# Optimization experiments

Hardware: AMD Instinct MI355X
Metric: run time of the kernel (lower is better)

## Reference

```python
import jax, jax.numpy as jnp
import numpy as np

B, S, D = 2, 1024, 512
E, K = 8, 2          # num_experts, top_k (hardcoded in EncoderLayerMOE)
HMOE = 4             # SMoE_MHA heads
HD = D // HMOE       # 128 head dim for local experts
HID = 4 * D          # 2048 expert hidden (both extractors)
AH = 4               # attention heads
DK = D // AH
NEG = -1e9


def layer_norm(x, w, b, eps=1e-12):
    mu = x.mean(-1, keepdims=True)
    var = ((x - mu) ** 2).mean(-1, keepdims=True)
    return (x - mu) * jax.lax.rsqrt(var + eps) * w + b


def moe(x, gate_w, gate_b, w1, b1, w2, b2):
    """Dense all-expert SMoE, gather top-k, re-softmax topk weights (faithful).
    x: [..., d]; w1: [E,d,H]; w2: [E,H,d]."""
    gate_scores = x @ gate_w + gate_b                      # [..., E]
    sm = jax.nn.softmax(gate_scores, axis=-1)
    topk_s, topk_i = jax.lax.top_k(sm, K)                  # [..., K]
    h1 = jax.nn.relu(jnp.einsum('...d,edh->...eh', x, w1) + b1)   # [..., E, H]
    out = jnp.einsum('...eh,ehd->...ed', h1, w2) + b2      # [..., E, d]
    idx = jnp.broadcast_to(topk_i[..., None], topk_i.shape + (out.shape[-1],))
    sel = jnp.take_along_axis(out, idx, axis=-2)           # [..., K, d]
    w = jax.nn.softmax(topk_s, axis=-1)[..., None]         # re-softmax of topk scores
    return (sel * w).sum(-2)


def local_extractor(x, pre_w, pre_b, gate_w, gate_b, w1, b1, w2, b2, align_w, align_b):
    b, s, d = x.shape
    xp = x @ pre_w + pre_b
    xf = xp.reshape(b, s, HMOE, HD).transpose(0, 2, 1, 3)  # [b,h,s,hd]
    eo = moe(xf, gate_w, gate_b, w1, b1, w2, b2)
    xf = xf + eo
    xo = xf.transpose(0, 2, 1, 3).reshape(b, s, d)
    return xo @ align_w + align_b


def mha(xq, xkv, mask, wq, bq, wk, bk, wv, bv, wo, bo):
    b, sq, d = xq.shape
    sk = xkv.shape[1]
    q = (xq @ wq + bq).reshape(b, sq, AH, DK).transpose(0, 2, 1, 3)
    k = (xkv @ wk + bk).reshape(b, sk, AH, DK).transpose(0, 2, 1, 3)
    v = (xkv @ wv + bv).reshape(b, sk, AH, DK).transpose(0, 2, 1, 3)
    scores = jnp.einsum('bhqd,bhkd->bhqk', q, k) / jnp.sqrt(jnp.float32(DK))
    m = mask[:, None, :, :]                                 # [b,1,1,sk]
    scores = jnp.where(m, scores, NEG)
    attn = jax.nn.softmax(scores, axis=-1)
    attn = jnp.where(m, attn, 0.0)
    o = jnp.einsum('bhqk,bhkd->bhqd', attn, v)
    o = o.transpose(0, 2, 1, 3).reshape(b, sq, d)
    return o @ wo + bo


def setup_inputs() -> dict:
    key = jax.random.key(0)
    ks = iter(jax.random.split(key, 64))
    def p(shape, scale=0.02):
        return (jax.random.normal(next(ks), shape, jnp.float32) * scale)
    z = lambda *s: jnp.zeros(s, jnp.float32)
    o = lambda *s: jnp.ones(s, jnp.float32)
    return dict(
        x=jax.random.normal(next(ks), (B, S, D), jnp.float32),
        pre_w=p((D, D)), pre_b=z(D),
        l_gate_w=p((HD, E)), l_gate_b=z(E),
        l_w1=p((E, HD, HID)), l_b1=z(E, HID),
        l_w2=p((E, HID, HD)), l_b2=z(E, HD),
        align_w=p((D, D)), align_b=z(D),
        ln1_w=o(D), ln1_b=z(D),
        wq=p((D, D)), bq=z(D), wk=p((D, D)), bk=z(D),
        wv=p((D, D)), bv=z(D), wo=p((D, D)), bo=z(D),
        ln2_w=o(D), ln2_b=z(D),
        g_gate_w=p((D, E)), g_gate_b=z(E),
        g_w1=p((E, D, HID)), g_b1=z(E, HID),
        g_w2=p((E, HID, D)), g_b2=z(E, D),
        mask=jnp.ones((B, 1, S), bool),
    )


def reference(x, pre_w, pre_b, l_gate_w, l_gate_b, l_w1, l_b1, l_w2, l_b2,
              align_w, align_b, ln1_w, ln1_b, wq, bq, wk, bk, wv, bv, wo, bo,
              ln2_w, ln2_b, g_gate_w, g_gate_b, g_w1, g_b1, g_w2, g_b2, mask):
    # EncoderLayerMOE.forward, eval mode, normalize_before=True, cache=None
    residual = x
    xl = local_extractor(x, pre_w, pre_b, l_gate_w, l_gate_b,
                         l_w1, l_b1, l_w2, l_b2, align_w, align_b)
    xn = layer_norm(xl, ln1_w, ln1_b)
    att = mha(xn, xn, mask, wq, bq, wk, bk, wv, bv, wo, bo)
    x1 = residual + att
    residual = x1
    x2 = layer_norm(x1, ln2_w, ln2_b)
    g = moe(x2, g_gate_w, g_gate_b, g_w1, g_b1, g_w2, g_b2)
    out = residual + g
    return out
```

## Files before the change

### kernel.cpp

```cpp
#include <hip/hip_runtime.h>

typedef unsigned short ushort_t;
typedef __attribute__((ext_vector_type(8))) short short8;
typedef __attribute__((ext_vector_type(4))) short short4v;
typedef __attribute__((ext_vector_type(4))) float f32x4;

constexpr int B_    = 2;
constexpr int S_    = 1024;
constexpr int D_    = 512;
constexpr int E_    = 8;
constexpr int HMOE_ = 4;
constexpr int HD_   = 128;
constexpr int HID_  = 2048;
constexpr int AH_   = 4;
constexpr int NTOK  = B_ * S_;
constexpr int NSUB  = B_ * HMOE_ * S_;

#define DEVINL __device__ __forceinline__

DEVINL ushort_t f2bf(float f) {
    union { float f; unsigned int i; } c;
    c.f = f;
    unsigned int x = c.i;
    return (ushort_t)((x + 0x7fffu + ((x >> 16) & 1u)) >> 16);
// ... 146 lines not shown

__global__ __launch_bounds__(256) void wconv_k(
    const float* __restrict__ in, ushort_t* __restrict__ out, int R, int C)
{
    __shared__ float tile[64][65];
    const int e = blockIdx.z;
    const int c0 = blockIdx.x * 64, r0 = blockIdx.y * 64;
    const float* src = in + ((size_t)e * R + r0) * C + c0;
    const int cl = threadIdx.x & 63, rl = threadIdx.x >> 6;
    #pragma unroll
    for (int j = 0; j < 16; j++) {
        int rr = rl * 16 + j;
        tile[rr][cl] = src[(size_t)rr * C + cl];
    }
    __syncthreads();
    ushort_t* dst = out + ((size_t)e * C + c0) * R + r0;
    #pragma unroll
    for (int j = 0; j < 16; j++) {
        int cc = rl * 16 + j;
        dst[(size_t)cc * R + cl] = f2bf(tile[cl][cc]);
    }
}

__global__ __launch_bounds__(256) void f2bf_k(
    const float* __restrict__ X, ushort_t* __restrict__ Y, int n)
{
    int i = (blockIdx.x * 256 + threadIdx.x) * 4;
    if (i < n) {
        float4 v = *reinterpret_cast<const float4*>(X + i);
        short4v o;
        o.x = (short)f2bf(v.x); o.y = (short)f2bf(v.y);
        o.z = (short)f2bf(v.z); o.w = (short)f2bf(v.w);
        *reinterpret_cast<short4v*>(Y + i) = o;
    }
}

__global__ __launch_bounds__(256) void vtrans_bf_k(
    const ushort_t* __restrict__ Vbf, ushort_t* __restrict__ VT)
{
    __shared__ ushort_t tile[64][68];
    const int s0 = blockIdx.x * 64;
    const int d0 = blockIdx.y * 64;
    const int bh = blockIdx.z;
    const int b = bh >> 2, h = bh & 3;
    const ushort_t* src = Vbf + (size_t)(b * S_ + s0) * D_ + h * HD_ + d0;
    const int cl = threadIdx.x & 63, rl = threadIdx.x >> 6;
    #pragma unroll
    for (int j = 0; j < 16; j++) {
        int rr = rl * 16 + j;
        tile[rr][cl] = src[(size_t)rr * D_ + cl];
    }
    __syncthreads();
    ushort_t* dst = VT + ((size_t)bh * HD_ + d0) * S_ + s0;
    #pragma unroll
    for (int j = 0; j < 16; j++) {
        int cc = rl * 16 + j;
        dst[(size_t)cc * S_ + cl] = tile[cl][cc];
    }
}

template <bool LOCAL>
__global__ __launch_bounds__(256) void gate_score_k(
    const float* __restrict__ X, const float* __restrict__ gwm,
    const float* __restrict__ gb, int2* __restrict__ choice,
    float2* __restrict__ cweight)
{
    constexpr int DIMD = LOCAL ? HD_ : D_;
    constexpr int PL = DIMD / 64;
    const int t = blockIdx.x * 4 + (threadIdx.x >> 6);
    const int lane = threadIdx.x & 63;
    const float* x = X + (LOCAL ? local_off(t) : (size_t)t * D_);
    float xr[PL];
    #pragma unroll
    for (int i = 0; i < PL; i++) xr[i] = x[lane + 64 * i];
    float sc[8];
    #pragma unroll
    for (int e = 0; e < 8; e++) {
        float a = 0.f;
        #pragma unroll
        for (int i = 0; i < PL; i++)
            a = fmaf(xr[i], gwm[(size_t)(lane + 64 * i) * E_ + e], a);
        #pragma unroll
        for (int o2 = 32; o2; o2 >>= 1) a += __shfl_xor(a, o2);
        sc[e] = a;
    }
    if (lane == 0) {
        float mx = -1e30f;
        #pragma unroll
        for (int e = 0; e < 8; e++) { sc[e] += gb[e]; mx = fmaxf(mx, sc[e]); }
        float p[8], psum = 0.f;
        #pragma unroll
        for (int e = 0; e < 8; e++) { p[e] = expf(sc[e] - mx); psum += p[e]; }
        float inv = 1.f / psum;
        #pragma unroll
        for (int e = 0; e < 8; e++) p[e] *= inv;
        int i0 = 0;
        for (int e = 1; e < 8; e++) if (p[e] > p[i0]) i0 = e;
        int i1 = (i0 == 0) ? 1 : 0;
        for (int e = 0; e < 8; e++) if (e != i0 && p[e] > p[i1]) i1 = e;
        float e0 = expf(p[i0]), e1 = expf(p[i1]);
        float wnorm = 1.f / (e0 + e1);
        choice[t]  = (int2){i0, i1};
        cweight[t] = (float2){e0 * wnorm, e1 * wnorm};
    }
}

template <int CAP>
__global__ __launch_bounds__(256) void gate_build_k(
    const int2* __restrict__ choice, const float2* __restrict__ cweight,
    int* __restrict__ cnt, int* __restrict__ idx, float* __restrict__ gwv)
{
    __shared__ int wtot[4];
    __shared__ int basesh;
    const int e = blockIdx.x;
    const int tid = threadIdx.x;
    const int lane = tid & 63, wv = tid >> 6;
    if (tid == 0) basesh = 0;
    __syncthreads();
    for (int t0 = 0; t0 < CAP; t0 += 256) {
        int t = t0 + tid;
        int2 ch = choice[t];
        float2 cw = cweight[t];
        bool m0 = (ch.x == e);
        bool m = m0 | (ch.y == e);
        float w = m0 ? cw.x : cw.y;
        unsigned long long mask = __ballot(m);
        int posw = __popcll(mask & ((1ull << lane) - 1ull));
        if (lane == 0) wtot[wv] = __popcll(mask);
        __syncthreads();
        int base = basesh;
        int woff = 0, tot = 0;
        #pragma unroll
        for (int i = 0; i < 4; i++) {
            int c = wtot[i];
            tot += c;
            if (i < wv) woff += c;
        }
        if (m) {
            int p = base + woff + posw;
            idx[e * CAP + p] = t;
            gwv[e * CAP + p] = w;
        }
        __syncthreads();
        if (tid == 0) basesh = base + tot;
    }
    __syncthreads();
    int total = basesh;
    if (tid == 0) cnt[e] = total;
    int padEnd = (total + 63) & ~63;
    if (padEnd > CAP) padEnd = CAP;
    for (int p = total + tid; p < padEnd; p += 256) {
        idx[e * CAP + p] = 0;
        gwv[e * CAP + p] = 0.f;
    }
}

template <int DIMD, int GSPLIT>
__global__ __launch_bounds__(256, 3) void ffn_grouped3_k(
    const ushort_t* __restrict__ Xbf,
    const ushort_t* __restrict__ w1t, const float* __restrict__ b1,
    const ushort_t* __restrict__ w2t, const float* __restrict__ b2,
    const int* __restrict__ cnt, const int* __restrict__ idx,
    const float* __restrict__ gwv, float* __restrict__ OUT)
{
    constexpr int K1  = DIMD;
    constexpr int NT2 = DIMD / 128;
    constexpr int CAP = (DIMD == HD_) ? NSUB : NTOK;
    constexpr int HC  = 128;
    constexpr int CHUNKS = HID_ / HC / GSPLIT;
    constexpr bool PIPE = (NT2 == 1);

    __shared__ ushort_t bufA[64 * 72];
    __shared__ ushort_t bufB[128 * 72];
    __shared__ ushort_t Hs[64 * 136];
    __shared__ float    gws[64];
    __shared__ size_t   toffs[64];

    const int tid  = threadIdx.x;
    const int lane = tid & 63;
    const int wv   = tid >> 6;
    const int e    = blockIdx.x & 7;
    const int rest = blockIdx.x >> 3;
    const int mt   = rest / GSPLIT;
    const int g    = rest % GSPLIT;
    const int m0   = mt * 64;

    if (m0 >= cnt[e]) return;

    if (tid < 64) {
        int t = idx[e * CAP + m0 + tid];
        toffs[tid] = (DIMD == HD_) ? local_off(t) : (size_t)t * D_;
        gws[tid]   = gwv[e * CAP + m0 + tid];
    }
    __syncthreads();

    const int l15 = lane & 15, l4 = lane >> 4;
    const int ar = tid >> 2, as = (tid & 3) * 16;
    const int bn = tid >> 1, bs = (tid & 1) * 32;

    f32x4 accO[NT2][4][2];
    #pragma unroll
    for (int n2 = 0; n2 < NT2; n2++)
        #pragma unroll
        for (int mi = 0; mi < 4; mi++)
            #pragma unroll
            for (int ni = 0; ni < 2; ni++)
                accO[n2][mi][ni] = (f32x4){0.f, 0.f, 0.f, 0.f};

    const ushort_t* w1e = w1t + (size_t)e * HID_ * K1;
    const ushort_t* w2e = w2t + (size_t)e * DIMD * HID_;
    const float* b1e = b1 + (size_t)e * HID_;

    short8 ra0, ra1, rb0, rb1, rb2, rb3;

    const int hc0 = g * CHUNKS * HC;
    for (int hc = hc0; hc < hc0 + CHUNKS * HC; hc += HC) {
        f32x4 acc1[4][2];
        #pragma unroll
        for (int mi = 0; mi < 4; mi++)
            #pragma unroll
            for (int ni = 0; ni < 2; ni++)
                acc1[mi][ni] = (f32x4){0.f, 0.f, 0.f, 0.f};

        if (PIPE) {
            const ushort_t* xp = Xbf + toffs[ar] + as;
            ra0 = *reinterpret_cast<const short8*>(xp);
            ra1 = *reinterpret_cast<const short8*>(xp + 8);
            const ushort_t* wp = w1e + (size_t)(hc + bn) * K1 + bs;
            rb0 = *reinterpret_cast<const short8*>(wp);
            rb1 = *reinterpret_cast<const short8*>(wp + 8);
            rb2 = *reinterpret_cast<const short8*>(wp + 16);
            rb3 = *reinterpret_cast<const short8*>(wp + 24);
        }

        for (int k0 = 0; k0 < K1; k0 += 64) {
            __syncthreads();
            if (PIPE) {
                ushort_t* dst = &bufA[ar * 72 + as];
                *reinterpret_cast<short8*>(dst)     = ra0;
                *reinterpret_cast<short8*>(dst + 8) = ra1;
                ushort_t* dstb = &bufB[bn * 72 + bs];
                *reinterpret_cast<short8*>(dstb)      = rb0;
                *reinterpret_cast<short8*>(dstb + 8)  = rb1;
                *reinterpret_cast<short8*>(dstb + 16) = rb2;
                *reinterpret_cast<short8*>(dstb + 24) = rb3;
                if (k0 + 64 < K1) {
                    const ushort_t* xp = Xbf + toffs[ar] + k0 + 64 + as;
                    ra0 = *reinterpret_cast<const short8*>(xp);
                    ra1 = *reinterpret_cast<const short8*>(xp + 8);
                    const ushort_t* wp = w1e + (size_t)(hc + bn) * K1 + k0 + 64 + bs;
                    rb0 = *reinterpret_cast<const short8*>(wp);
                    rb1 = *reinterpret_cast<const short8*>(wp + 8);
                    rb2 = *reinterpret_cast<const short8*>(wp + 16);
                    rb3 = *reinterpret_cast<const short8*>(wp + 24);
                }
            } else {
                {
                    const ushort_t* xp = Xbf + toffs[ar] + k0 + as;
                    ushort_t* dst = &bufA[ar * 72 + as];
                    *reinterpret_cast<short8*>(dst)     = *reinterpret_cast<const short8*>(xp);
                    *reinterpret_cast<short8*>(dst + 8) = *reinterpret_cast<const short8*>(xp + 8);
                }
                {
                    const ushort_t* wp = w1e + (size_t)(hc + bn) * K1 + k0 + bs;
                    ushort_t* dst = &bufB[bn * 72 + bs];
                    #pragma unroll
                    for (int j = 0; j < 32; j += 8)
                        *reinterpret_cast<short8*>(dst + j) = *reinterpret_cast<const short8*>(wp + j);
                }
            }
            __syncthreads();
            #pragma unroll
            for (int ks = 0; ks < 2; ks++) {
                short8 af[4], bfr[2];
                #pragma unroll
                for (int mi = 0; mi < 4; mi++)
                    af[mi] = *reinterpret_cast<const short8*>(&bufA[(mi * 16 + l15) * 72 + ks * 32 + l4 * 8]);
                #pragma unroll
                for (int ni = 0; ni < 2; ni++)
                    bfr[ni] = *reinterpret_cast<const short8*>(&bufB[(wv * 32 + ni * 16 + l15) * 72 + ks * 32 + l4 * 8]);
                #pragma unroll
                for (int mi = 0; mi < 4; mi++)
                    #pragma unroll
                    for (int ni = 0; ni < 2; ni++)
                        acc1[mi][ni] = __builtin_amdgcn_mfma_f32_16x16x32_bf16(
                            af[mi], bfr[ni], acc1[mi][ni], 0, 0, 0);
            }
        }

        if (PIPE) {
            const ushort_t* wp = w2e + (size_t)bn * HID_ + hc + bs;
            rb0 = *reinterpret_cast<const short8*>(wp);
            rb1 = *reinterpret_cast<const short8*>(wp + 8);
            rb2 = *reinterpret_cast<const short8*>(wp + 16);
            rb3 = *reinterpret_cast<const short8*>(wp + 24);
        }

        float b1v0 = b1e[hc + wv * 32 + l15];
        float b1v1 = b1e[hc + wv * 32 + 16 + l15];
        #pragma unroll
        for (int mi = 0; mi < 4; mi++)
            #pragma unroll
            for (int ni = 0; ni < 2; ni++) {
                float bb = (ni == 0) ? b1v0 : b1v1;
                #pragma unroll
                for (int r = 0; r < 4; r++) {
                    int row = mi * 16 + l4 * 4 + r;
                    int col = wv * 32 + ni * 16 + l15;
                    Hs[row * 136 + col] = f2bf(fmaxf(acc1[mi][ni][r] + bb, 0.f));
                }
            }

        #pragma unroll
        for (int n2 = 0; n2 < NT2; n2++) {
            #pragma unroll
            for (int k2t = 0; k2t < 2; k2t++) {
                __syncthreads();
                if (PIPE) {
                    ushort_t* dst = &bufB[bn * 72 + bs];
                    *reinterpret_cast<short8*>(dst)      = rb0;
                    *reinterpret_cast<short8*>(dst + 8)  = rb1;
                    *reinterpret_cast<short8*>(dst + 16) = rb2;
                    *reinterpret_cast<short8*>(dst + 24) = rb3;
                    if (!(n2 == NT2 - 1 && k2t == 1)) {
                        int nn2 = (k2t == 1) ? n2 + 1 : n2;
                        int nk  = (k2t == 1) ? 0 : 1;
                        const ushort_t* wp = w2e + (size_t)(nn2 * 128 + bn) * HID_ + hc + nk * 64 + bs;
                        rb0 = *reinterpret_cast<const short8*>(wp);
                        rb1 = *reinterpret_cast<const short8*>(wp + 8);
                        rb2 = *reinterpret_cast<const short8*>(wp + 16);
                        rb3 = *reinterpret_cast<const short8*>(wp + 24);
                    }
                } else {
                    const ushort_t* wp = w2e + (size_t)(n2 * 128 + bn) * HID_ + hc + k2t * 64 + bs;
                    ushort_t* dst = &bufB[bn * 72 + bs];
                    #pragma unroll
                    for (int j = 0; j < 32; j += 8)
                        *reinterpret_cast<short8*>(dst + j) = *reinterpret_cast<const short8*>(wp + j);
                }
                __syncthreads();
                #pragma unroll
                for (int ks = 0; ks < 2; ks++) {
                    short8 af[4], bfr[2];
                    #pragma unroll
                    for (int mi = 0; mi < 4; mi++)
                        af[mi] = *reinterpret_cast<const short8*>(&Hs[(mi * 16 + l15) * 136 + k2t * 64 + ks * 32 + l4 * 8]);
                    #pragma unroll
                    for (int ni = 0; ni < 2; ni++)
                        bfr[ni] = *reinterpret_cast<const short8*>(&bufB[(wv * 32 + ni * 16 + l15) * 72 + ks * 32 + l4 * 8]);
                    #pragma unroll
                    for (int mi = 0; mi < 4; mi++)
                        #pragma unroll
                        for (int ni = 0; ni < 2; ni++)
                            accO[n2][mi][ni] = __builtin_amdgcn_mfma_f32_16x16x32_bf16(
                                af[mi], bfr[ni], accO[n2][mi][ni], 0, 0, 0);
                }
            }
        }
    }

    #pragma unroll
    for (int n2 = 0; n2 < NT2; n2++) {
        float b2v0 = (g == 0) ? b2[(size_t)e * DIMD + n2 * 128 + wv * 32 + l15] : 0.f;
        float b2v1 = (g == 0) ? b2[(size_t)e * DIMD + n2 * 128 + wv * 32 + 16 + l15] : 0.f;
        #pragma unroll
        for (int mi = 0; mi < 4; mi++)
            #pragma unroll
            for (int r = 0; r < 4; r++) {
                int row = mi * 16 + l4 * 4 + r;
                float gg = gws[row];
                if (gg != 0.f) {
                    float* op = OUT + toffs[row] + n2 * 128 + wv * 32;
                    atomicAdd(op + l15,      gg * (accO[n2][mi][0][r] + b2v0));
                    atomicAdd(op + 16 + l15, gg * (accO[n2][mi][1][r] + b2v1));
                }
            }
    }
}

template <int DIMD>
__global__ __launch_bounds__(256) void ffn_grouped_k(
    const float* __restrict__ Xf,
    const float* __restrict__ w1f, const float* __restrict__ b1,
    const float* __restrict__ w2f, const float* __restrict__ b2,
    const int* __restrict__ cnt, const int* __restrict__ idx,
    const float* __restrict__ gwv, float* __restrict__ OUT)
{
    constexpr int K1  = DIMD;
    constexpr int NT2 = DIMD / 128;
    constexpr int CAP = (DIMD == HD_) ? NSUB : NTOK;
    constexpr int HC  = 128;

    __shared__ ushort_t bufB[128 * 72];
    __shared__ ushort_t bufA[128 * 72];
    __shared__ ushort_t Hs[64 * 136];
    __shared__ float    gws[64];
    __shared__ size_t   toffs[64];

    const int tid  = threadIdx.x;
    const int lane = tid & 63;
    const int wv   = tid >> 6;
    const int e    = blockIdx.x & 7;
    const int rest = blockIdx.x >> 3;
    const int mt   = (NT2 == 1) ? rest : (rest >> 2);
    const int n2b  = (NT2 == 1) ? 0 : (rest & 3) * 128;
    const int m0   = mt * 64;

    if (m0 >= cnt[e]) return;

    if (tid < 64) {
        int t = idx[e * CAP + m0 + tid];
        toffs[tid] = (DIMD == HD_) ? local_off(t) : (size_t)t * D_;
        gws[tid]   = gwv[e * CAP + m0 + tid];
    }
    __syncthreads();

    const int l15 = lane & 15, l4 = lane >> 4;

    f32x4 accO[4][2];
    #pragma unroll
    for (int mi = 0; mi < 4; mi++)
        #pragma unroll
        for (int ni = 0; ni < 2; ni++)
            accO[mi][ni] = (f32x4){0.f, 0.f, 0.f, 0.f};

    const float* w1e_f = w1f + (size_t)e * K1 * HID_;
    const float* w2e_f = w2f + (size_t)e * HID_ * DIMD;
    const float* b1e = b1 + (size_t)e * HID_;

    for (int hc = 0; hc < HID_; hc += HC) {
        f32x4 acc1[4][2];
        #pragma unroll
        for (int mi = 0; mi < 4; mi++)
            #pragma unroll
            for (int ni = 0; ni < 2; ni++)
                acc1[mi][ni] = (f32x4){0.f, 0.f, 0.f, 0.f};

        for (int k0 = 0; k0 < K1; k0 += 64) {
            __syncthreads();
            {
                int r = tid >> 2, sg = (tid & 3) * 16;
                const float* xp = Xf + toffs[r] + k0 + sg;
                ushort_t* dst = &bufA[r * 72 + sg];
                #pragma unroll
                for (int j = 0; j < 16; j += 4) {
                    float4 v = *reinterpret_cast<const float4*>(xp + j);
                    dst[j + 0] = f2bf(v.x); dst[j + 1] = f2bf(v.y);
                    dst[j + 2] = f2bf(v.z); dst[j + 3] = f2bf(v.w);
                }
            }
            {
                int kk = tid >> 2, ns = (tid & 3) * 32;
                const float* wp = w1e_f + (size_t)(k0 + kk) * HID_ + hc + ns;
                #pragma unroll
                for (int j = 0; j < 32; j += 4) {
                    float4 v = *reinterpret_cast<const float4*>(wp + j);
                    bufB[(ns + j + 0) * 72 + kk] = f2bf(v.x);
                    bufB[(ns + j + 1) * 72 + kk] = f2bf(v.y);
                    bufB[(ns + j + 2) * 72 + kk] = f2bf(v.z);
                    bufB[(ns + j + 3) * 72 + kk] = f2bf(v.w);
                }
            }
            __syncthreads();
            #pragma unroll
            for (int ks = 0; ks < 2; ks++) {
                short8 af[4], bfr[2];
                #pragma unroll
                for (int mi = 0; mi < 4; mi++)
                    af[mi] = *reinterpret_cast<const short8*>(&bufA[(mi * 16 + l15) * 72 + ks * 32 + l4 * 8]);
                #pragma unroll
                for (int ni = 0; ni < 2; ni++)
                    bfr[ni] = *reinterpret_cast<const short8*>(&bufB[(wv * 32 + ni * 16 + l15) * 72 + ks * 32 + l4 * 8]);
                #pragma unroll
                for (int mi = 0; mi < 4; mi++)
                    #pragma unroll
                    for (int ni = 0; ni < 2; ni++)
                        acc1[mi][ni] = __builtin_amdgcn_mfma_f32_16x16x32_bf16(
                            af[mi], bfr[ni], acc1[mi][ni], 0, 0, 0);
            }
        }

        float b1v0 = b1e[hc + wv * 32 + l15];
        float b1v1 = b1e[hc + wv * 32 + 16 + l15];
        #pragma unroll
        for (int mi = 0; mi < 4; mi++)
            #pragma unroll
            for (int ni = 0; ni < 2; ni++) {
                float bb = (ni == 0) ? b1v0 : b1v1;
                #pragma unroll
                for (int r = 0; r < 4; r++) {
                    int row = mi * 16 + l4 * 4 + r;
                    int col = wv * 32 + ni * 16 + l15;
                    Hs[row * 136 + col] = f2bf(fmaxf(acc1[mi][ni][r] + bb, 0.f));
                }
            }

        #pragma unroll
        for (int k2t = 0; k2t < 2; k2t++) {
            __syncthreads();
            {
                int kk = tid >> 2, ns = (tid & 3) * 32;
                const float* wp = w2e_f + (size_t)(hc + k2t * 64 + kk) * DIMD + n2b + ns;
                #pragma unroll
                for (int j = 0; j < 32; j += 4) {
                    float4 v = *reinterpret_cast<const float4*>(wp + j);
                    bufA[(ns + j + 0) * 72 + kk] = f2bf(v.x);
                    bufA[(ns + j + 1) * 72 + kk] = f2bf(v.y);
                    bufA[(ns + j + 2) * 72 + kk] = f2bf(v.z);
                    bufA[(ns + j + 3) * 72 + kk] = f2bf(v.w);
                }
            }
            __syncthreads();
            #pragma unroll
            for (int ks = 0; ks < 2; ks++) {
                short8 af[4], bfr[2];
                #pragma unroll
                for (int mi = 0; mi < 4; mi++)
                    af[mi] = *reinterpret_cast<const short8*>(&Hs[(mi * 16 + l15) * 136 + k2t * 64 + ks * 32 + l4 * 8]);
                #pragma unroll
                for (int ni = 0; ni < 2; ni++)
                    bfr[ni] = *reinterpret_cast<const short8*>(&bufA[(wv * 32 + ni * 16 + l15) * 72 + ks * 32 + l4 * 8]);
                #pragma unroll
                for (int mi = 0; mi < 4; mi++)
                    #pragma unroll
                    for (int ni = 0; ni < 2; ni++)
                        accO[mi][ni] = __builtin_amdgcn_mfma_f32_16x16x32_bf16(
                            af[mi], bfr[ni], accO[mi][ni], 0, 0, 0);
            }
        }
    }

    float b2v0 = b2[(size_t)e * DIMD + n2b + wv * 32 + l15];
// ... 189 lines not shown

    for (int kc = 0; kc < S_; kc += KC) {
        for (int i = tid * 4; i < KC * 128; i += 1024) {
            int r = i >> 7, c = i & 127;
            float4 v = *reinterpret_cast<const float4*>(Kb + base + (size_t)(kc + r) * D_ + c);
            kst[c + 0][r] = v.x; kst[c + 1][r] = v.y;
            kst[c + 2][r] = v.z; kst[c + 3][r] = v.w;
        }
        __syncthreads();

        {
            float s[2][4] = {};
            #pragma unroll 8
            for (int d = 0; d < 128; d++) {
                float a0 = qsT[d][sy * 2];
                float a1 = qsT[d][sy * 2 + 1];
                float4 kb4 = *reinterpret_cast<const float4*>(&kst[d][sx * 4]);
                s[0][0] = fmaf(a0, kb4.x, s[0][0]); s[0][1] = fmaf(a0, kb4.y, s[0][1]);
                s[0][2] = fmaf(a0, kb4.z, s[0][2]); s[0][3] = fmaf(a0, kb4.w, s[0][3]);
                s[1][0] = fmaf(a1, kb4.x, s[1][0]); s[1][1] = fmaf(a1, kb4.y, s[1][1]);
                s[1][2] = fmaf(a1, kb4.z, s[1][2]); s[1][3] = fmaf(a1, kb4.w, s[1][3]);
            }
            #pragma unroll
            for (int j = 0; j < 4; j++) {
                psT[sx * 4 + j][sy * 2]     = s[0][j];
                psT[sx * 4 + j][sy * 2 + 1] = s[1][j];
            }
        }
        __syncthreads();

        {
            int r = tid >> 3, c0 = (tid & 7) * 8;
            float vals[8];
            float mx = -1e30f;
            #pragma unroll
            for (int j = 0; j < 8; j++) { vals[j] = psT[c0 + j][r]; mx = fmaxf(mx, vals[j]); }
            mx = fmaxf(mx, __shfl_xor(mx, 1));
            mx = fmaxf(mx, __shfl_xor(mx, 2));
            mx = fmaxf(mx, __shfl_xor(mx, 4));
            float mold = mrow[r];
            float mnew = fmaxf(mold, mx);
            float alpha = __expf(mold - mnew);
            float sum = 0.f;
            #pragma unroll
            for (int j = 0; j < 8; j++) {
                float pexp = __expf(vals[j] - mnew);
                psT[c0 + j][r] = pexp;
                sum += pexp;
            }
            sum += __shfl_xor(sum, 1);
            sum += __shfl_xor(sum, 2);
            sum += __shfl_xor(sum, 4);
            if ((tid & 7) == 0) { mrow[r] = mnew; lrow[r] = lrow[r] * alpha + sum; arow[r] = alpha; }
        }
        __syncthreads();

        {
            #pragma unroll
            for (int i2 = 0; i2 < 4; i2++) {
                float al = arow[py * 4 + i2];
                #pragma unroll
                for (int j = 0; j < 4; j++) o[i2][j] *= al;
            }
            #pragma unroll 4
            for (int k = 0; k < KC; k++) {
                float4 pv = *reinterpret_cast<const float4*>(&psT[k][py * 4]);
                float4 vv = *reinterpret_cast<const float4*>(V + base + (size_t)(kc + k) * D_ + px * 4);
                float pa[4] = {pv.x, pv.y, pv.z, pv.w};
                #pragma unroll
                for (int i2 = 0; i2 < 4; i2++) {
                    o[i2][0] = fmaf(pa[i2], vv.x, o[i2][0]);
                    o[i2][1] = fmaf(pa[i2], vv.y, o[i2][1]);
                    o[i2][2] = fmaf(pa[i2], vv.z, o[i2][2]);
                    o[i2][3] = fmaf(pa[i2], vv.w, o[i2][3]);
                }
            }
        }
        __syncthreads();
    }

    #pragma unroll
    for (int i2 = 0; i2 < 4; i2++) {
        float inv = 1.f / lrow[py * 4 + i2];
        float4 ov;
        ov.x = o[i2][0] * inv; ov.y = o[i2][1] * inv;
        ov.z = o[i2][2] * inv; ov.w = o[i2][3] * inv;
        *reinterpret_cast<float4*>(AO + base + (size_t)(q0 + py * 4 + i2) * D_ + px * 4) = ov;
    }
}

__global__ __launch_bounds__(256) void copy_out_k(
    const float* __restrict__ X, float* __restrict__ Y, int n)
{
    int base = (blockIdx.x * 256 + threadIdx.x) * 4;
    if (base < n)
        *reinterpret_cast<float4*>(Y + base) = *reinterpret_cast<const float4*>(X + base);
}

extern "C" void kernel_launch(void* const* d_in, const int* in_sizes, int n_in,
                              void* d_out, int out_size, void* d_ws, size_t ws_size,
                              hipStream_t stream)
{
    (void)in_sizes; (void)n_in; (void)out_size;
    const float* x        = (const float*)d_in[0];
    const float* pre_w    = (const float*)d_in[1];
    const float* pre_b    = (const float*)d_in[2];
    const float* l_gate_w = (const float*)d_in[3];
    const float* l_gate_b = (const float*)d_in[4];
    const float* l_w1     = (const float*)d_in[5];
    const float* l_b1     = (const float*)d_in[6];
    const float* l_w2     = (const float*)d_in[7];
    const float* l_b2     = (const float*)d_in[8];
    const float* align_w  = (const float*)d_in[9];
    const float* align_b  = (const float*)d_in[10];
    const float* ln1_w    = (const float*)d_in[11];
    const float* ln1_b    = (const float*)d_in[12];
    const float* wq       = (const float*)d_in[13];
    const float* bq       = (const float*)d_in[14];
    const float* wk       = (const float*)d_in[15];
    const float* bk       = (const float*)d_in[16];
    const float* wv       = (const float*)d_in[17];
    const float* bv       = (const float*)d_in[18];
    const float* wo       = (const float*)d_in[19];
    const float* bo       = (const float*)d_in[20];
    const float* ln2_w    = (const float*)d_in[21];
    const float* ln2_b    = (const float*)d_in[22];
    const float* g_gate_w = (const float*)d_in[23];
    const float* g_gate_b = (const float*)d_in[24];
    const float* g_w1     = (const float*)d_in[25];
    const float* g_b1     = (const float*)d_in[26];
    const float* g_w2     = (const float*)d_in[27];
    const float* g_b2     = (const float*)d_in[28];

    char* ws = (char*)d_ws;
    const size_t MB  = 1024 * 1024;
    const size_t MB4 = (size_t)NTOK * D_ * sizeof(float);
    float* W0 = (float*)(ws + 0 * MB);
    float* W1 = (float*)(ws + 4 * MB);
    float* W2 = (float*)(ws + 8 * MB);

    const bool pre = ws_size >= (size_t)59 * MB;

    char* blob = ws + (pre ? 12 : 16) * MB;
    int*    cntl = (int*)(blob);
    int*    cntg = (int*)(blob + 32);
    int*    idxl = (int*)(blob + 64);
    int*    idxg = (int*)(blob + 64 + 262144);
    float*  gwvl = (float*)(blob + 64 + 262144 + 65536);
    float*  gwvg = (float*)(blob + 64 + 262144 + 65536 + 262144);
    int2*   chl  = (int2*)(blob + 64 + 262144 + 65536 + 262144 + 65536);
    float2* cwl  = (float2*)((char*)chl + 65536);
    int2*   chg  = (int2*)((char*)cwl + 65536);
    float2* cwg  = (float2*)((char*)chg + 16384);

    ushort_t* x_bf = (ushort_t*)(ws + 12 * MB);
    ushort_t* preT   = (ushort_t*)(ws + 14 * MB);
    ushort_t* alignT = (ushort_t*)(ws + 14 * MB + 512 * 1024);
    ushort_t* wqT    = (ushort_t*)(ws + 15 * MB);
    ushort_t* wkT    = (ushort_t*)(ws + 15 * MB + 512 * 1024);
    ushort_t* wvT    = (ushort_t*)(ws + 16 * MB);
    ushort_t* woT    = (ushort_t*)(ws + 16 * MB + 512 * 1024);
    ushort_t* XBF  = (ushort_t*)(ws + 17 * MB);
    ushort_t* Vbf  = (ushort_t*)(ws + 4 * MB);
    ushort_t* VTb  = (ushort_t*)(ws + 6 * MB);
    ushort_t* Qbf  = (ushort_t*)(ws + 8 * MB);
    ushort_t* Kbf  = (ushort_t*)(ws + 10 * MB);
    ushort_t* LW1T = (ushort_t*)(ws + 19 * MB);
    ushort_t* LW2T = (ushort_t*)(ws + 23 * MB);
    ushort_t* GW1T = (ushort_t*)(ws + 27 * MB);
    ushort_t* GW2T = (ushort_t*)(ws + 43 * MB);
    float* W3 = (float*)(ws + 12 * MB);

    const dim3 gg(D_ / 64, NTOK / 64);

    if (pre) {
        f2bf_k<<<(NTOK * D_) / (256 * 4), 256, 0, stream>>>(x, x_bf, NTOK * D_);
        wconv_k<<<dim3(8, 8, 1), 256, 0, stream>>>(pre_w,   preT,   D_, D_);
        wconv_k<<<dim3(8, 8, 1), 256, 0, stream>>>(align_w, alignT, D_, D_);
        wconv_k<<<dim3(8, 8, 1), 256, 0, stream>>>(wq, wqT, D_, D_);
        wconv_k<<<dim3(8, 8, 1), 256, 0, stream>>>(wk, wkT, D_, D_);
        wconv_k<<<dim3(8, 8, 1), 256, 0, stream>>>(wv, wvT, D_, D_);
        wconv_k<<<dim3(8, 8, 1), 256, 0, stream>>>(wo, woT, D_, D_);
        wconv_k<<<dim3(HID_ / 64, HD_ / 64, 8),  256, 0, stream>>>(l_w1, LW1T, HD_,  HID_);
        wconv_k<<<dim3(HD_ / 64,  HID_ / 64, 8), 256, 0, stream>>>(l_w2, LW2T, HID_, HD_);
        wconv_k<<<dim3(HID_ / 64, D_ / 64, 8),   256, 0, stream>>>(g_w1, GW1T, D_,   HID_);
        wconv_k<<<dim3(D_ / 64,   HID_ / 64, 8), 256, 0, stream>>>(g_w2, GW2T, HID_, D_);

        gemm_mfma_k<true, true, false><<<gg, 256, 0, stream>>>(x_bf, preT, pre_b, nullptr, W0, XBF);
        gate_score_k<true><<<NSUB / 4, 256, 0, stream>>>(W0, l_gate_w, l_gate_b, chl, cwl);
        gate_build_k<NSUB><<<8, 256, 0, stream>>>(chl, cwl, cntl, idxl, gwvl);
        hipMemcpyAsync(W1, W0, MB4, hipMemcpyDeviceToDevice, stream);
        ffn_grouped3_k<HD_, 4><<<8 * (NSUB / 64) * 4, 256, 0, stream>>>(
            XBF, LW1T, l_b1, LW2T, l_b2, cntl, idxl, gwvl, W1);
        f2bf_k<<<(NTOK * D_) / (256 * 4), 256, 0, stream>>>(W1, XBF, NTOK * D_);
        gemm_mfma_k<true, false, false><<<gg, 256, 0, stream>>>(XBF, alignT, align_b, nullptr, W2, nullptr);
        ln_k<false, true><<<NTOK, 256, 0, stream>>>(W2, ln1_w, ln1_b, W0, XBF);
        gemm_mfma_k<false, true, false><<<gg, 256, 0, stream>>>(XBF, wqT, bq, nullptr, nullptr, Qbf);
        gemm_mfma_k<false, true, false><<<gg, 256, 0, stream>>>(XBF, wkT, bk, nullptr, nullptr, Kbf);
        gemm_mfma_k<false, true, false><<<gg, 256, 0, stream>>>(XBF, wvT, bv, nullptr, nullptr, Vbf);
        vtrans_bf_k<<<dim3(16, 2, 8), 256, 0, stream>>>(Vbf, VTb);
        fattn_mfma_k<<<dim3(S_ / 32, B_ * AH_), 256, 0, stream>>>(Qbf, Kbf, VTb, XBF);
        gemm_mfma_k<true, false, true><<<gg, 256, 0, stream>>>(XBF, woT, bo, x, W0, nullptr);
        ln_k<true, true><<<NTOK, 256, 0, stream>>>(W0, ln2_w, ln2_b, W2, XBF);
        gate_score_k<false><<<NTOK / 4, 256, 0, stream>>>(W2, g_gate_w, g_gate_b, chg, cwg);
        gate_build_k<NTOK><<<8, 256, 0, stream>>>(chg, cwg, cntg, idxg, gwvg);
        ffn_grouped3_k<D_, 8><<<8 * (NTOK / 64) * 8, 256, 0, stream>>>(
            XBF, GW1T, g_b1, GW2T, g_b2, cntg, idxg, gwvg, W0);
        copy_out_k<<<(NTOK * D_) / (256 * 4), 256, 0, stream>>>(W0, (float*)d_out, NTOK * D_);
    } else {
        gemm_bias_k<false><<<gg, 256, 0, stream>>>(x, pre_w, pre_b, nullptr, W0, NTOK, D_, D_);
        gate_score_k<true><<<NSUB / 4, 256, 0, stream>>>(W0, l_gate_w, l_gate_b, chl, cwl);
        gate_build_k<NSUB><<<8, 256, 0, stream>>>(chl, cwl, cntl, idxl, gwvl);
        hipMemcpyAsync(W1, W0, MB4, hipMemcpyDeviceToDevice, stream);
        ffn_grouped_k<HD_><<<8 * (NSUB / 64), 256, 0, stream>>>(
            W0, l_w1, l_b1, l_w2, l_b2, cntl, idxl, gwvl, W1);
        gemm_bias_k<false><<<gg, 256, 0, stream>>>(W1, align_w, align_b, nullptr, W2, NTOK, D_, D_);
        ln_k<true, false><<<NTOK, 256, 0, stream>>>(W2, ln1_w, ln1_b, W0, nullptr);
        gemm_bias_k<false><<<gg, 256, 0, stream>>>(W0, wq, bq, nullptr, W1, NTOK, D_, D_);
        gemm_bias_k<false><<<gg, 256, 0, stream>>>(W0, wk, bk, nullptr, W2, NTOK, D_, D_);
        gemm_bias_k<false><<<gg, 256, 0, stream>>>(W0, wv, bv, nullptr, W3, NTOK, D_, D_);
        fattn_k<<<dim3(S_ / QT, B_ * AH_), 256, 0, stream>>>(W1, W2, W3, W1);
        gemm_bias_k<true><<<gg, 256, 0, stream>>>(W1, wo, bo, x, W0, NTOK, D_, D_);
        ln_k<true, false><<<NTOK, 256, 0, stream>>>(W0, ln2_w, ln2_b, W2, nullptr);
        gate_score_k<false><<<NTOK / 4, 256, 0, stream>>>(W2, g_gate_w, g_gate_b, chg, cwg);
        gate_build_k<NTOK><<<8, 256, 0, stream>>>(chg, cwg, cntg, idxg, gwvg);
        ffn_grouped_k<D_><<<8 * (NTOK / 64) * 4, 256, 0, stream>>>(
            W2, g_w1, g_b1, g_w2, g_b2, cntg, idxg, gwvg, W0);
        copy_out_k<<<(NTOK * D_) / (256 * 4), 256, 0, stream>>>(W0, (float*)d_out, NTOK * D_);
    }
}
```

Measured before the change: 507.8 us.

## Split global MoE FFN into two-stage grouped GEMMs with materialized hidden buffer

Replaces the fused per-expert FFN kernel for the global MoE with separate up-projection and down-projection grouped GEMM kernels. A prefix kernel computes per-expert slot offsets, and the ReLU hidden activations are stored in bf16 to a workspace buffer in two 1024-wide hidden halves. The intent is to drop the recompute and GSPLIT partitioning of the fused kernel and improve tile occupancy. In exchange it adds global-memory traffic for the hidden buffer, extra launches, and a second round of atomic adds into the output.

```diff
diff --git a/kernel.cpp b/kernel.cpp
--- a/kernel.cpp
+++ b/kernel.cpp
@@ -322,6 +322,14 @@
     for (int p = total + tid; p < padEnd; p += 256) {
         idx[e * CAP + p] = 0;
         gwv[e * CAP + p] = 0.f;
+    }
+}
+
+__global__ void prefix_k(const int* __restrict__ cnt, int* __restrict__ prefix)
+{
+    if (threadIdx.x == 0) {
+        int s = 0;
+        for (int e = 0; e < 8; e++) { prefix[e] = s; s += cnt[e]; }
     }
 }
 
@@ -548,6 +556,228 @@
     }
 }
 
+__global__ __launch_bounds__(256) void ffn1g_k(
+    const ushort_t* __restrict__ Xbf,
+    const ushort_t* __restrict__ w1t, const float* __restrict__ b1,
+    const int* __restrict__ cnt, const int* __restrict__ prefix,
+    const int* __restrict__ idx, int hbase, ushort_t* __restrict__ Hbuf)
+{
+    __shared__ ushort_t bufA[64 * 72];
+    __shared__ ushort_t bufB[128 * 72];
+    __shared__ size_t   toffs[64];
+    __shared__ int      sbase;
+
+    const int tid  = threadIdx.x;
+    const int lane = tid & 63;
+    const int wv   = tid >> 6;
+    const int e    = blockIdx.x & 7;
+    const int rest = blockIdx.x >> 3;
+    const int mt   = rest >> 3;
+    const int hs   = rest & 7;
+    const int m0   = mt * 64;
+    const int ce   = cnt[e];
+    if (m0 >= ce) return;
+
+    if (tid < 64) toffs[tid] = (size_t)idx[e * NTOK + m0 + tid] * D_;
+    if (tid == 0) sbase = prefix[e];
+    __syncthreads();
+
+    const int l15 = lane & 15, l4 = lane >> 4;
+    const int ar = tid >> 2, as = (tid & 3) * 16;
+    const int bn = tid >> 1, bs = (tid & 1) * 32;
+    const int hc = hbase + hs * 128;
+
+    const ushort_t* w1e = w1t + (size_t)e * HID_ * D_;
+
+    f32x4 acc1[4][2];
+    #pragma unroll
+    for (int mi = 0; mi < 4; mi++)
+        #pragma unroll
+        for (int ni = 0; ni < 2; ni++)
+            acc1[mi][ni] = (f32x4){0.f, 0.f, 0.f, 0.f};
+
+    short8 ra0, ra1, rb0, rb1, rb2, rb3;
+    {
+        const ushort_t* xp = Xbf + toffs[ar] + as;
+        ra0 = *reinterpret_cast<const short8*>(xp);
+        ra1 = *reinterpret_cast<const short8*>(xp + 8);
+        const ushort_t* wp = w1e + (size_t)(hc + bn) * D_ + bs;
+        rb0 = *reinterpret_cast<const short8*>(wp);
+        rb1 = *reinterpret_cast<const short8*>(wp + 8);
+        rb2 = *reinterpret_cast<const short8*>(wp + 16);
+        rb3 = *reinterpret_cast<const short8*>(wp + 24);
+    }
+    for (int k0 = 0; k0 < D_; k0 += 64) {
+        __syncthreads();
+        {
+            ushort_t* dst = &bufA[ar * 72 + as];
+            *reinterpret_cast<short8*>(dst)     = ra0;
+            *reinterpret_cast<short8*>(dst + 8) = ra1;
+            ushort_t* dstb = &bufB[bn * 72 + bs];
+            *reinterpret_cast<short8*>(dstb)      = rb0;
+            *reinterpret_cast<short8*>(dstb + 8)  = rb1;
+            *reinterpret_cast<short8*>(dstb + 16) = rb2;
+            *reinterpret_cast<short8*>(dstb + 24) = rb3;
+        }
+        if (k0 + 64 < D_) {
+            const ushort_t* xp = Xbf + toffs[ar] + k0 + 64 + as;
+            ra0 = *reinterpret_cast<const short8*>(xp);
+            ra1 = *reinterpret_cast<const short8*>(xp + 8);
+            const ushort_t* wp = w1e + (size_t)(hc + bn) * D_ + k0 + 64 + bs;
+            rb0 = *reinterpret_cast<const short8*>(wp);
+            rb1 = *reinterpret_cast<const short8*>(wp + 8);
+            rb2 = *reinterpret_cast<const short8*>(wp + 16);
+            rb3 = *reinterpret_cast<const short8*>(wp + 24);
+        }
+        __syncthreads();
+        #pragma unroll
+        for (int ks = 0; ks < 2; ks++) {
+            short8 af[4], bfr[2];
+            #pragma unroll
+            for (int mi = 0; mi < 4; mi++)
+                af[mi] = *reinterpret_cast<const short8*>(&bufA[(mi * 16 + l15) * 72 + ks * 32 + l4 * 8]);
+            #pragma unroll
+            for (int ni = 0; ni < 2; ni++)
+                bfr[ni] = *reinterpret_cast<const short8*>(&bufB[(wv * 32 + ni * 16 + l15) * 72 + ks * 32 + l4 * 8]);
+            #pragma unroll
+            for (int mi = 0; mi < 4; mi++)
+                #pragma unroll
+                for (int ni = 0; ni < 2; ni++)
+                    acc1[mi][ni] = __builtin_amdgcn_mfma_f32_16x16x32_bf16(
+                        af[mi], bfr[ni], acc1[mi][ni], 0, 0, 0);
+        }
+    }
+
+    const int slotbase = sbase + m0;
+    const int hout = (hc - hbase);
+    float b1v0 = b1[(size_t)e * HID_ + hc + wv * 32 + l15];
+    float b1v1 = b1[(size_t)e * HID_ + hc + wv * 32 + 16 + l15];
+    #pragma unroll
+    for (int mi = 0; mi < 4; mi++)
+        #pragma unroll
+        for (int ni = 0; ni < 2; ni++) {
+            float bb = (ni == 0) ? b1v0 : b1v1;
+            #pragma unroll
+            for (int r = 0; r < 4; r++) {
+                int row = mi * 16 + l4 * 4 + r;
+                if (m0 + row < ce) {
+                    int col = hout + wv * 32 + ni * 16 + l15;
+                    Hbuf[(size_t)(slotbase + row) * 1024 + col] =
+                        f2bf(fmaxf(acc1[mi][ni][r] + bb, 0.f));
+                }
+            }
+        }
+}
+
+template <bool ADD_B2>
+__global__ __launch_bounds__(256) void ffn2g_k(
+    const ushort_t* __restrict__ Hbuf,
+    const ushort_t* __restrict__ w2t, const float* __restrict__ b2,
+    const int* __restrict__ cnt, const int* __restrict__ prefix,
+    const int* __restrict__ idx, const float* __restrict__ gwv,
+    int hbase, float* __restrict__ OUT)
+{
+    __shared__ ushort_t bufA[32 * 72];
+    __shared__ ushort_t bufB[128 * 72];
+    __shared__ float    gws[32];
+    __shared__ size_t   toffs[32];
+    __shared__ int      sbase;
+
+    const int tid  = threadIdx.x;
+    const int lane = tid & 63;
+    const int wv   = tid >> 6;
+    const int e    = blockIdx.x & 7;
+    const int rest = blockIdx.x >> 3;
+    const int mt   = rest >> 2;
+    const int n2   = rest & 3;
+    const int m0   = mt * 32;
+    const int ce   = cnt[e];
+    if (m0 >= ce) return;
+
+    if (tid < 32) {
+        toffs[tid] = (size_t)idx[e * NTOK + m0 + tid] * D_;
+        gws[tid]   = gwv[e * NTOK + m0 + tid];
+    }
+    if (tid == 0) sbase = prefix[e];
+    __syncthreads();
+
+    const int l15 = lane & 15, l4 = lane >> 4;
+    const int ar = tid >> 3, as = (tid & 7) * 8;
+    const int bn = tid >> 1, bs = (tid & 1) * 32;
+    const int slot0 = sbase + m0;
+
+    const ushort_t* w2e = w2t + (size_t)e * D_ * HID_;
+    const ushort_t* Hb  = Hbuf + (size_t)slot0 * 1024;
+
+    f32x4 acc[2][2];
+    #pragma unroll
+    for (int mi = 0; mi < 2; mi++)
+        #pragma unroll
+        for (int ni = 0; ni < 2; ni++)
+            acc[mi][ni] = (f32x4){0.f, 0.f, 0.f, 0.f};
+
+    short8 ra0, rb0, rb1, rb2, rb3;
+    {
+        ra0 = *reinterpret_cast<const short8*>(Hb + (size_t)ar * 1024 + as);
+        const ushort_t* wp = w2e + (size_t)(n2 * 128 + bn) * HID_ + hbase + bs;
+        rb0 = *reinterpret_cast<const short8*>(wp);
+        rb1 = *reinterpret_cast<const short8*>(wp + 8);
+        rb2 = *reinterpret_cast<const short8*>(wp + 16);
+        rb3 = *reinterpret_cast<const short8*>(wp + 24);
+    }
+    for (int k0 = 0; k0 < 1024; k0 += 64) {
+        __syncthreads();
+        {
+            *reinterpret_cast<short8*>(&bufA[ar * 72 + as]) = ra0;
+            ushort_t* dstb = &bufB[bn * 72 + bs];
+            *reinterpret_cast<short8*>(dstb)      = rb0;
+            *reinterpret_cast<short8*>(dstb + 8)  = rb1;
+            *reinterpret_cast<short8*>(dstb + 16) = rb2;
+            *reinterpret_cast<short8*>(dstb + 24) = rb3;
+        }
+        if (k0 + 64 < 1024) {
+            ra0 = *reinterpret_cast<const short8*>(Hb + (size_t)ar * 1024 + k0 + 64 + as);
+            const ushort_t* wp = w2e + (size_t)(n2 * 128 + bn) * HID_ + hbase + k0 + 64 + bs;
+            rb0 = *reinterpret_cast<const short8*>(wp);
+            rb1 = *reinterpret_cast<const short8*>(wp + 8);
+            rb2 = *reinterpret_cast<const short8*>(wp + 16);
+            rb3 = *reinterpret_cast<const short8*>(wp + 24);
+        }
+        __syncthreads();
+        #pragma unroll
+        for (int ks = 0; ks < 2; ks++) {
+            short8 af[2], bfr[2];
+            #pragma unroll
+            for (int mi = 0; mi < 2; mi++)
+                af[mi] = *reinterpret_cast<const short8*>(&bufA[(mi * 16 + l15) * 72 + ks * 32 + l4 * 8]);
+            #pragma unroll
+            for (int ni = 0; ni < 2; ni++)
+                bfr[ni] = *reinterpret_cast<const short8*>(&bufB[(wv * 32 + ni * 16 + l15) * 72 + ks * 32 + l4 * 8]);
+            #pragma unroll
+            for (int mi = 0; mi < 2; mi++)
+                #pragma unroll
+                for (int ni = 0; ni < 2; ni++)
+                    acc[mi][ni] = __builtin_amdgcn_mfma_f32_16x16x32_bf16(
+                        af[mi], bfr[ni], acc[mi][ni], 0, 0, 0);
+        }
+    }
+
+    float b2v0 = ADD_B2 ? b2[(size_t)e * D_ + n2 * 128 + wv * 32 + l15] : 0.f;
+    float b2v1 = ADD_B2 ? b2[(size_t)e * D_ + n2 * 128 + wv * 32 + 16 + l15] : 0.f;
+    #pragma unroll
+    for (int mi = 0; mi < 2; mi++)
+        #pragma unroll
+        for (int r = 0; r < 4; r++) {
+            int row = mi * 16 + l4 * 4 + r;
+            float g = gws[row];
+            if (g != 0.f) {
+                float* op = OUT + toffs[row] + n2 * 128 + wv * 32;
+                atomicAdd(op + l15,      g * (acc[mi][0][r] + b2v0));
+                atomicAdd(op + 16 + l15, g * (acc[mi][1][r] + b2v1));
+            }
+        }
+}
+
 template <int DIMD>
 __global__ __launch_bounds__(256) void ffn_grouped_k(
     const float* __restrict__ Xf,
@@ -1043,6 +1273,7 @@
     float2* cwl  = (float2*)((char*)chl + 65536);
     int2*   chg  = (int2*)((char*)cwl + 65536);
     float2* cwg  = (float2*)((char*)chg + 16384);
+    int*    prefg = (int*)((char*)cwg + 16384);
 
     ushort_t* x_bf = (ushort_t*)(ws + 12 * MB);
     ushort_t* preT   = (ushort_t*)(ws + 14 * MB);
@@ -1056,6 +1287,7 @@
     ushort_t* VTb  = (ushort_t*)(ws + 6 * MB);
     ushort_t* Qbf  = (ushort_t*)(ws + 8 * MB);
     ushort_t* Kbf  = (ushort_t*)(ws + 10 * MB);
+    ushort_t* Hbuf = (ushort_t*)(ws + 4 * MB);
     ushort_t* LW1T = (ushort_t*)(ws + 19 * MB);
     ushort_t* LW2T = (ushort_t*)(ws + 23 * MB);
     ushort_t* GW1T = (ushort_t*)(ws + 27 * MB);
@@ -1095,8 +1327,15 @@
         ln_k<true, true><<<NTOK, 256, 0, stream>>>(W0, ln2_w, ln2_b, W2, XBF);
         gate_score_k<false><<<NTOK / 4, 256, 0, stream>>>(W2, g_gate_w, g_gate_b, chg, cwg);
         gate_build_k<NTOK><<<8, 256, 0, stream>>>(chg, cwg, cntg, idxg, gwvg);
-        ffn_grouped3_k<D_, 8><<<8 * (NTOK / 64) * 8, 256, 0, stream>>>(
-            XBF, GW1T, g_b1, GW2T, g_b2, cntg, idxg, gwvg, W0);
+        prefix_k<<<1, 64, 0, stream>>>(cntg, prefg);
+        ffn1g_k<<<8 * 32 * 8, 256, 0, stream>>>(
+            XBF, GW1T, g_b1, cntg, prefg, idxg, 0, Hbuf);
+        ffn2g_k<true><<<8 * 64 * 4, 256, 0, stream>>>(
+            Hbuf, GW2T, g_b2, cntg, prefg, idxg, gwvg, 0, W0);
+        ffn1g_k<<<8 * 32 * 8, 256, 0, stream>>>(
+            XBF, GW1T, g_b1, cntg, prefg, idxg, 1024, Hbuf);
+        ffn2g_k<false><<<8 * 64 * 4, 256, 0, stream>>>(
+            Hbuf, GW2T, g_b2, cntg, prefg, idxg, gwvg, 1024, W0);
         copy_out_k<<<(NTOK * D_) / (256 * 4), 256, 0, stream>>>(W0, (float*)d_out, NTOK * D_);
     } else {
         gemm_bias_k<false><<<gg, 256, 0, stream>>>(x, pre_w, pre_b, nullptr, W0, NTOK, D_, D_);
```

Result: faster. 468.6 us (-7.7%).
